# Kernel tuning notes

Hardware: AMD Instinct MI355X
Metric: run time of the kernel (lower is better)

The kernel has to match this reference:

```python
import jax, jax.numpy as jnp
import numpy as np

NUM_RELS = 64
EDGES_PER_REL = 16384
N_NODES = 100000
IN_FEAT = 128
OUT_FEAT = 128
NUM_BASES = 16
E = NUM_RELS * EDGES_PER_REL


def setup_inputs() -> dict:
    key = jax.random.key(0)
    ks = jax.random.split(key, 8)
    feat = jax.random.normal(ks[0], (N_NODES, IN_FEAT), dtype=jnp.float32)
    weight = jax.random.normal(ks[1], (NUM_BASES, IN_FEAT, OUT_FEAT), dtype=jnp.float32) * 0.05
    w_comp = jax.random.normal(ks[2], (NUM_RELS, NUM_BASES), dtype=jnp.float32) * 0.3
    h_bias = jnp.zeros((OUT_FEAT,), dtype=jnp.float32)
    loop_weight = jax.random.normal(ks[3], (IN_FEAT, OUT_FEAT), dtype=jnp.float32) * 0.05
    norm = jax.random.uniform(ks[4], (E, 1), dtype=jnp.float32)
    src = jax.random.randint(ks[5], (E,), 0, N_NODES, dtype=jnp.int32).astype(jnp.int64)
    dst = jax.random.randint(ks[6], (E,), 0, N_NODES, dtype=jnp.int32).astype(jnp.int64)
    # edges are sorted by relation type with uniform per-relation sections
    etypes = jnp.repeat(jnp.arange(NUM_RELS, dtype=jnp.int64), EDGES_PER_REL)
    return {"feat": feat, "weight": weight, "w_comp": w_comp, "h_bias": h_bias,
            "loop_weight": loop_weight, "norm": norm, "src": src, "dst": dst,
            "etypes": etypes, "section": EDGES_PER_REL}


def reference(feat, weight, w_comp, h_bias, loop_weight, norm, src, dst, etypes, section):
    num_rels, num_bases = w_comp.shape
    n_nodes, in_feat = feat.shape
    out_feat = weight.shape[2]
    # basis composition: per-relation weights [R, in, out]
    W = jnp.matmul(w_comp, weight.reshape(num_bases, in_feat * out_feat))
    W = W.reshape(num_rels, in_feat, out_feat)
    # gather per-edge source features (edges sorted by relation, uniform sections)
    h_e = feat[src]                                   # [E, in]
    n_edges = h_e.shape[0]
    h_r = h_e.reshape(num_rels, section, in_feat)     # [R, e_r, in]
    msg = jnp.einsum('rei,rio->reo', h_r, W)          # grouped matmul
    msg = msg.reshape(n_edges, out_feat) * norm       # edge-norm scaling
    # scatter-sum aggregation to destination nodes
    node_repr = jax.ops.segment_sum(msg, dst, num_segments=n_nodes)
    node_repr = node_repr + h_bias + jnp.matmul(feat, loop_weight)
    return jax.nn.relu(node_repr)
```

## Files before the change

### kernel.cpp

```cpp
#include <hip/hip_runtime.h>

#define N_NODES 100000
#define N_PAD 100352
#define NBLK 392
#define IN_FEAT 128
#define OUT_FEAT 128
#define NUM_RELS 64
#define EDGES_PER_REL 16384
#define NUM_BASES 16
#define E_TOTAL (NUM_RELS * EDGES_PER_REL)

typedef __bf16 bf16x8 __attribute__((ext_vector_type(8)));
typedef float floatx4 __attribute__((ext_vector_type(4)));

__global__ __launch_bounds__(256) void compose_w_bf16_kernel(
    const float* __restrict__ weight, const float* __restrict__ w_comp,
    __bf16* __restrict__ Wp) {
  int idx = blockIdx.x * 256 + threadIdx.x;
  int r = idx >> 14;
  int off = idx & 16383;
  int j = off & 7, n = (off >> 3) & 127, kp = off >> 10;
  int k = kp * 8 + j;
  const float* wc = w_comp + r * NUM_BASES;
  float acc = 0.f;
#pragma unroll
  for (int b = 0; b < NUM_BASES; ++b)
    acc += wc[b] * weight[b * 16384 + k * 128 + n];
  Wp[idx] = (__bf16)acc;
}

__global__ __launch_bounds__(256) void pack_loop_w_kernel(
    const float* __restrict__ loop_w, __bf16* __restrict__ Lp) {
  int idx = blockIdx.x * 256 + threadIdx.x;
  int j = idx & 7, n = (idx >> 3) & 127, kp = idx >> 10;
  Lp[idx] = (__bf16)loop_w[(kp * 8 + j) * 128 + n];
}

__global__ __launch_bounds__(256) void compose_w_f32_kernel(
    const float* __restrict__ weight, const float* __restrict__ w_comp,
    float* __restrict__ W) {
  int idx = blockIdx.x * 256 + threadIdx.x;
  int r = idx >> 14;
  int io = idx & 16383;
  const float* wc = w_comp + r * NUM_BASES;
  float acc = 0.f;
#pragma unroll
  for (int b = 0; b < NUM_BASES; ++b)
    acc += wc[b] * weight[b * 16384 + io];
  W[idx] = acc;
}

__global__ __launch_bounds__(256) void init_out_mfma(
    const float* __restrict__ feat, const __bf16* __restrict__ Lp,
    const float* __restrict__ bias, float* __restrict__ out) {
  __shared__ __bf16 A_lds[64 * 136];
  int t = threadIdx.x;
  long base = (long)blockIdx.x * 64;
#pragma unroll
  for (int j = 0; j < 8; ++j) {
    int idx = t + j * 256;
    int e = idx >> 5, k4 = idx & 31;
    long n = base + e;
    float4 v = make_float4(0.f, 0.f, 0.f, 0.f);
    if (n < N_NODES) v = ((const float4*)feat)[n * 32 + k4];
    __bf16 tb[4] = {(__bf16)v.x, (__bf16)v.y, (__bf16)v.z, (__bf16)v.w};
    *(ushort4*)&A_lds[e * 136 + k4 * 4] = *(ushort4*)tb;
  }
  __syncthreads();

  int wave = t >> 6, lane = t & 63;
  int m16 = lane & 15, quad = lane >> 4;
  floatx4 acc[8];
#pragma unroll
  for (int nt = 0; nt < 8; ++nt) acc[nt] = (floatx4){0.f, 0.f, 0.f, 0.f};

  const __bf16* a_base = &A_lds[(wave * 16 + m16) * 136 + quad * 8];
#pragma unroll
  for (int ks = 0; ks < 4; ++ks) {
    bf16x8 a = *(const bf16x8*)(a_base + ks * 32);
    int kp = ks * 4 + quad;
#pragma unroll
    for (int nt = 0; nt < 8; ++nt) {
      bf16x8 b = *(const bf16x8*)(Lp + (kp * 128 + nt * 16 + m16) * 8);
      acc[nt] = __builtin_amdgcn_mfma_f32_16x16x32_bf16(a, b, acc[nt], 0, 0, 0);
    }
  }

  float bv[8];
#pragma unroll
  for (int nt = 0; nt < 8; ++nt) bv[nt] = bias[nt * 16 + m16];
#pragma unroll
  for (int r = 0; r < 4; ++r) {
    long n = base + wave * 16 + quad * 4 + r;
    if (n < N_NODES) {
#pragma unroll
      for (int nt = 0; nt < 8; ++nt)
        out[n * 128 + nt * 16 + m16] = acc[nt][r] + bv[nt];
    }
  }
}

__global__ __launch_bounds__(256) void zero_kernel(int* __restrict__ p) {
  p[blockIdx.x * 256 + threadIdx.x] = 0;
}

__global__ __launch_bounds__(256) void hist8_kernel(
    const int* __restrict__ dst, int* __restrict__ cnt8, int cshift) {
  int e = blockIdx.x * 256 + threadIdx.x;
  int c = e >> cshift;
  atomicAdd(&cnt8[c * N_PAD + dst[e]], 1);
}

__global__ __launch_bounds__(256) void scan1_kernel(
    const int* __restrict__ cnt, int* __restrict__ row,
    int* __restrict__ bsum) {
  __shared__ int s[256];
  int t = threadIdx.x;
  int idx = blockIdx.x * 256 + t;
  int v = cnt[idx];
  s[t] = v;
  __syncthreads();
  for (int o = 1; o < 256; o <<= 1) {
    int x = (t >= o) ? s[t - o] : 0;
    __syncthreads();
    s[t] += x;
    __syncthreads();
  }
  row[idx] = s[t] - v;
  if (t == 255) bsum[blockIdx.x] = s[t];
}

__global__ __launch_bounds__(512) void scan2_kernel(
    const int* __restrict__ bsum, int* __restrict__ boff) {
  __shared__ int s[512];
  int t = threadIdx.x;
  int v = (t < NBLK) ? bsum[blockIdx.x * NBLK + t] : 0;
  s[t] = v;
  __syncthreads();
  for (int o = 1; o < 512; o <<= 1) {
    int x = (t >= o) ? s[t - o] : 0;
    __syncthreads();
    s[t] += x;
    __syncthreads();
  }
  if (t < NBLK) boff[blockIdx.x * NBLK + t] = s[t] - v;
}

__global__ __launch_bounds__(256) void scan3_kernel(
    int* __restrict__ row, const int* __restrict__ boff,
    int* __restrict__ fill) {
  int idx = blockIdx.x * 256 + threadIdx.x;
  int v = row[idx] + boff[blockIdx.x];
  row[idx] = v;
  fill[idx] = v;
}

__global__ __launch_bounds__(256) void scatter_pos_kernel(
    const int* __restrict__ dst, int* __restrict__ fill8,
    int* __restrict__ pos, int cshift) {
  int e = blockIdx.x * 256 + threadIdx.x;
  int c = e >> cshift;
  pos[e] = atomicAdd(&fill8[c * N_PAD + dst[e]], 1);
}

__global__ __launch_bounds__(256) void edge_gemm_mfma(
    const float* __restrict__ feat, const __bf16* __restrict__ Wp,
    const float* __restrict__ norm, const int* __restrict__ src,
    const int* __restrict__ pos, unsigned short* __restrict__ msg, int e_lo) {
  __shared__ __bf16 A_lds[64 * 136];
  __shared__ int s_src[64];
  __shared__ int s_pos[64];
  __shared__ float s_norm[64];
  int t = threadIdx.x;
  long base = (long)e_lo + (long)blockIdx.x * 64;
  int rel = (int)(base >> 14);
  const __bf16* Wr = Wp + (long)rel * (IN_FEAT * OUT_FEAT);

  if (t < 64) {
    s_src[t] = src[base + t];
    s_pos[t] = pos[base + t];
    s_norm[t] = norm[base + t];
  }
  __syncthreads();
#pragma unroll
  for (int j = 0; j < 8; ++j) {
    int idx = t + j * 256;
    int e = idx >> 5, k4 = idx & 31;
    float4 v = ((const float4*)feat)[(long)s_src[e] * 32 + k4];
    __bf16 tb[4] = {(__bf16)v.x, (__bf16)v.y, (__bf16)v.z, (__bf16)v.w};
    *(ushort4*)&A_lds[e * 136 + k4 * 4] = *(ushort4*)tb;
  }
  __syncthreads();

  int wave = t >> 6, lane = t & 63;
  int m16 = lane & 15, quad = lane >> 4;
  floatx4 acc[8];
#pragma unroll
  for (int nt = 0; nt < 8; ++nt) acc[nt] = (floatx4){0.f, 0.f, 0.f, 0.f};

  const __bf16* a_base = &A_lds[(wave * 16 + m16) * 136 + quad * 8];
#pragma unroll
  for (int ks = 0; ks < 4; ++ks) {
    bf16x8 a = *(const bf16x8*)(a_base + ks * 32);
    int kp = ks * 4 + quad;
#pragma unroll
    for (int nt = 0; nt < 8; ++nt) {
      bf16x8 b = *(const bf16x8*)(Wr + (kp * 128 + nt * 16 + m16) * 8);
      acc[nt] = __builtin_amdgcn_mfma_f32_16x16x32_bf16(a, b, acc[nt], 0, 0, 0);
    }
  }

  __syncthreads();
#pragma unroll
  for (int r = 0; r < 4; ++r) {
    int erow = wave * 16 + quad * 4 + r;
    float nm = s_norm[erow];
#pragma unroll
    for (int nt = 0; nt < 8; ++nt)
      A_lds[erow * 136 + nt * 16 + m16] = (__bf16)(acc[nt][r] * nm);
  }
  __syncthreads();
#pragma unroll
  for (int it = 0; it < 4; ++it) {
    int idx = it * 256 + t;
    int row = idx >> 4, seg = idx & 15;
    uint4 v = *(const uint4*)&A_lds[row * 136 + seg * 8];
    *(uint4*)(msg + (long)s_pos[row] * 128 + seg * 8) = v;
  }
}

__global__ __launch_bounds__(256) void gather_csr_kernel(
    const unsigned short* __restrict__ msg, const int* __restrict__ rowc,
    float* __restrict__ out, int do_relu) {
  int wave = threadIdx.x >> 6, lane = threadIdx.x & 63;
  int n = blockIdx.x * 4 + wave;
  if (n >= N_NODES) return;
  int beg = rowc[n], end = rowc[n + 1];
  if (!do_relu && beg == end) return;
  int half = lane >> 5;
  int c4 = lane & 31;
  float s0 = 0.f, s1 = 0.f, s2 = 0.f, s3 = 0.f;
  for (int j = beg + half; j < end; j += 2) {
    uint2 m = *(const uint2*)(msg + (long)j * 128 + c4 * 4);
    s0 += __uint_as_float(m.x << 16);
    s1 += __uint_as_float(m.x & 0xFFFF0000u);
    s2 += __uint_as_float(m.y << 16);
    s3 += __uint_as_float(m.y & 0xFFFF0000u);
  }
  s0 += __shfl_down(s0, 32);
  s1 += __shfl_down(s1, 32);
  s2 += __shfl_down(s2, 32);
  s3 += __shfl_down(s3, 32);
  if (half == 0) {
    float4 o = ((float4*)out)[(long)n * 32 + c4];
    o.x += s0; o.y += s1; o.z += s2; o.w += s3;
    if (do_relu) {
      o.x = fmaxf(o.x, 0.f); o.y = fmaxf(o.y, 0.f);
      o.z = fmaxf(o.z, 0.f); o.w = fmaxf(o.w, 0.f);
    }
    ((float4*)out)[(long)n * 32 + c4] = o;
  }
}

__global__ __launch_bounds__(256) void init_out_f32_kernel(
    const float* __restrict__ feat, const float* __restrict__ loop_w,
    const float* __restrict__ bias, float* __restrict__ out) {
  __shared__ float4 A4[64][32];
  int t = threadIdx.x;
  long base = (long)blockIdx.x * 64;
#pragma unroll
  for (int j = 0; j < 8; ++j) {
    int idx = t + j * 256;
    int e = idx >> 5, k4 = idx & 31;
    long n = base + e;
    float4 v = make_float4(0.f, 0.f, 0.f, 0.f);
    if (n < N_NODES) v = ((const float4*)feat)[n * 32 + k4];
    A4[e][k4] = v;
  }
  __syncthreads();
  int og = t & 31, eg = t >> 5;
  float acc[8][4];
#pragma unroll
  for (int j = 0; j < 8; ++j)
#pragma unroll
    for (int d = 0; d < 4; ++d) acc[j][d] = 0.f;
  const float4* W4 = (const float4*)loop_w;
  for (int k4 = 0; k4 < 32; ++k4) {
    float4 a[8];
#pragma unroll
    for (int j = 0; j < 8; ++j) a[j] = A4[eg * 8 + j][k4];
#pragma unroll
    for (int d = 0; d < 4; ++d) {
      float4 w = W4[(k4 * 4 + d) * 32 + og];
#pragma unroll
      for (int j = 0; j < 8; ++j) {
        float av = ((const float*)&a[j])[d];
        acc[j][0] += av * w.x;
        acc[j][1] += av * w.y;
        acc[j][2] += av * w.z;
        acc[j][3] += av * w.w;
      }
    }
  }
  float4 b = ((const float4*)bias)[og];
#pragma unroll
  for (int j = 0; j < 8; ++j) {
    long n = base + eg * 8 + j;
    if (n < N_NODES) {
      float4 v = make_float4(acc[j][0] + b.x, acc[j][1] + b.y,
                             acc[j][2] + b.z, acc[j][3] + b.w);
      ((float4*)out)[n * 32 + og] = v;
    }
  }
}

__global__ __launch_bounds__(256) void edge_msg_atomic_kernel(
    const float* __restrict__ feat, const float* __restrict__ W,
    const float* __restrict__ norm, const int* __restrict__ src,
    const int* __restrict__ dst, float* __restrict__ out) {
  __shared__ float4 A4[64][32];
  __shared__ int s_src[64];
  __shared__ int s_dst[64];
  __shared__ float s_norm[64];
  int t = threadIdx.x;
  long base = (long)blockIdx.x * 64;
  int rel = blockIdx.x >> 8;
  const float4* Wr4 = (const float4*)(W + (long)rel * IN_FEAT * OUT_FEAT);
  if (t < 64) {
    s_src[t] = src[base + t];
    s_dst[t] = dst[base + t];
    s_norm[t] = norm[base + t];
  }
  __syncthreads();
#pragma unroll
  for (int j = 0; j < 8; ++j) {
    int idx = t + j * 256;
    int e = idx >> 5, k4 = idx & 31;
    A4[e][k4] = ((const float4*)feat)[(long)s_src[e] * 32 + k4];
  }
  __syncthreads();
  int og = t & 31, eg = t >> 5;
  float acc[8][4];
#pragma unroll
  for (int j = 0; j < 8; ++j)
#pragma unroll
    for (int d = 0; d < 4; ++d) acc[j][d] = 0.f;
  for (int k4 = 0; k4 < 32; ++k4) {
    float4 a[8];
#pragma unroll
    for (int j = 0; j < 8; ++j) a[j] = A4[eg * 8 + j][k4];
#pragma unroll
    for (int d = 0; d < 4; ++d) {
      float4 w = Wr4[(k4 * 4 + d) * 32 + og];
#pragma unroll
      for (int j = 0; j < 8; ++j) {
        float av = ((const float*)&a[j])[d];
        acc[j][0] += av * w.x;
        acc[j][1] += av * w.y;
        acc[j][2] += av * w.z;
        acc[j][3] += av * w.w;
      }
    }
  }
#pragma unroll
  for (int j = 0; j < 8; ++j) {
    int e = eg * 8 + j;
    float nm = s_norm[e];
    float* orow = out + (long)s_dst[e] * OUT_FEAT + og * 4;
#pragma unroll
    for (int d = 0; d < 4; ++d) atomicAdd(orow + d, acc[j][d] * nm);
  }
}

__global__ __launch_bounds__(256) void relu_kernel(float* __restrict__ out) {
  int idx = blockIdx.x * 256 + threadIdx.x;
  float4 v = ((const float4*)out)[idx];
  v.x = fmaxf(v.x, 0.f);
  v.y = fmaxf(v.y, 0.f);
  v.z = fmaxf(v.z, 0.f);
  v.w = fmaxf(v.w, 0.f);
  ((float4*)out)[idx] = v;
}

extern "C" void kernel_launch(void* const* d_in, const int* in_sizes, int n_in,
                              void* d_out, int out_size, void* d_ws, size_t ws_size,
                              hipStream_t stream) {
  const float* feat   = (const float*)d_in[0];
  const float* weight = (const float*)d_in[1];
  const float* w_comp = (const float*)d_in[2];
  const float* h_bias = (const float*)d_in[3];
  const float* loop_w = (const float*)d_in[4];
  const float* norm   = (const float*)d_in[5];
  const int*   src    = (const int*)d_in[6];
  const int*   dst    = (const int*)d_in[7];
  float* out = (float*)d_out;

  const size_t SZ_WP  = (size_t)NUM_RELS * IN_FEAT * OUT_FEAT * 2;
  const size_t SZ_LP  = (size_t)IN_FEAT * OUT_FEAT * 2;
  const size_t SZ_POS = (size_t)E_TOTAL * 4;

  int CH = 0;
  {
    const int cands[4] = {32, 16, 8, 4};
    for (int i = 0; i < 4 && CH == 0; ++i) {
      int ch = cands[i], nc = NUM_RELS / ch;
      size_t need = SZ_WP + SZ_LP + SZ_POS + 2 * (size_t)nc * N_PAD * 4 +
                    2 * (size_t)nc * NBLK * 4 +
                    (size_t)ch * EDGES_PER_REL * OUT_FEAT * 2;
      if (ws_size >= need) CH = ch;
    }
  }

  if (CH > 0) {
    const int NC = NUM_RELS / CH;
    const int chunk_edges = CH * EDGES_PER_REL;
    int cshift = 14;
    for (int x = CH; x > 1; x >>= 1) ++cshift;

    char* p = (char*)d_ws;
    __bf16* Wp = (__bf16*)p;                  p += SZ_WP;
    __bf16* Lp = (__bf16*)p;                  p += SZ_LP;
    int* pos  = (int*)p;                      p += SZ_POS;
    int* cnt8 = (int*)p;                      p += (size_t)NC * N_PAD * 4;
    int* row8 = (int*)p;                      p += (size_t)NC * N_PAD * 4;
    int* bsum = (int*)p;                      p += (size_t)NC * NBLK * 4;
    int* boff = (int*)p;                      p += (size_t)NC * NBLK * 4;
    unsigned short* msg = (unsigned short*)p;

    hipLaunchKernelGGL(pack_loop_w_kernel, dim3(16384 / 256), dim3(256), 0,
                       stream, loop_w, Lp);
    hipLaunchKernelGGL(init_out_mfma, dim3((N_NODES + 63) / 64), dim3(256), 0,
                       stream, feat, Lp, h_bias, out);
    hipLaunchKernelGGL(compose_w_bf16_kernel, dim3(NUM_RELS * 16384 / 256),
                       dim3(256), 0, stream, weight, w_comp, Wp);
    hipLaunchKernelGGL(zero_kernel, dim3(NC * NBLK), dim3(256), 0, stream, cnt8);
    hipLaunchKernelGGL(hist8_kernel, dim3(E_TOTAL / 256), dim3(256), 0, stream,
                       dst, cnt8, cshift);
    hipLaunchKernelGGL(scan1_kernel, dim3(NC * NBLK), dim3(256), 0, stream,
                       cnt8, row8, bsum);
    hipLaunchKernelGGL(scan2_kernel, dim3(NC), dim3(512), 0, stream, bsum, boff);
    hipLaunchKernelGGL(scan3_kernel, dim3(NC * NBLK), dim3(256), 0, stream,
                       row8, boff, cnt8);
    hipLaunchKernelGGL(scatter_pos_kernel, dim3(E_TOTAL / 256), dim3(256), 0,
                       stream, dst, cnt8, pos, cshift);

    for (int c = 0; c < NC; ++c) {
      hipLaunchKernelGGL(edge_gemm_mfma, dim3(chunk_edges / 64), dim3(256), 0,
                         stream, feat, Wp, norm, src, pos, msg,
                         c * chunk_edges);
      hipLaunchKernelGGL(gather_csr_kernel, dim3((N_NODES + 3) / 4), dim3(256),
                         0, stream, msg, row8 + (size_t)c * N_PAD, out,
                         (c == NC - 1) ? 1 : 0);
    }
  } else {
    float* W = (float*)d_ws;
    hipLaunchKernelGGL(init_out_f32_kernel, dim3((N_NODES + 63) / 64),
                       dim3(256), 0, stream, feat, loop_w, h_bias, out);
    hipLaunchKernelGGL(compose_w_f32_kernel, dim3(NUM_RELS * 16384 / 256),
                       dim3(256), 0, stream, weight, w_comp, W);
    hipLaunchKernelGGL(edge_msg_atomic_kernel, dim3(E_TOTAL / 64), dim3(256), 0,
                       stream, feat, W, norm, src, dst, out);
    hipLaunchKernelGGL(relu_kernel, dim3((N_NODES * OUT_FEAT / 4) / 256),
                       dim3(256), 0, stream, out);
  }
}
```

Baseline: 460.1 us.

## Fuse edge GEMM with previous chunk's gather in double-buffered launches

Merges the edge GEMM and the CSR gather into one kernel whose blocks are interleaved by role. Each launch runs the GEMM for chunk d while gathering chunk d-1 from a second message buffer, so the two phases overlap on the GPU. The separate scatter_pos pass and its position array are removed by computing slot positions with atomics inside the GEMM blocks. Message stores and loads now use nontemporal hints. Chunks are smaller (max 16 relations) so two buffers fit in the workspace, which means more launches, and the kernel needs registers for both roles, which may lower occupancy.

```diff
diff --git a/kernel.cpp b/kernel.cpp
--- a/kernel.cpp
+++ b/kernel.cpp
@@ -9,9 +9,12 @@
 #define EDGES_PER_REL 16384
 #define NUM_BASES 16
 #define E_TOTAL (NUM_RELS * EDGES_PER_REL)
+#define GATHER_NBLK ((N_NODES + 3) / 4)
 
 typedef __bf16 bf16x8 __attribute__((ext_vector_type(8)));
 typedef float floatx4 __attribute__((ext_vector_type(4)));
+typedef unsigned int uint32x4 __attribute__((ext_vector_type(4)));
+typedef unsigned int uint32x2 __attribute__((ext_vector_type(2)));
 
 __global__ __launch_bounds__(256) void compose_w_bf16_kernel(
     const float* __restrict__ weight, const float* __restrict__ w_comp,
@@ -155,110 +158,115 @@
   fill[idx] = v;
 }
 
-__global__ __launch_bounds__(256) void scatter_pos_kernel(
-    const int* __restrict__ dst, int* __restrict__ fill8,
-    int* __restrict__ pos, int cshift) {
-  int e = blockIdx.x * 256 + threadIdx.x;
-  int c = e >> cshift;
-  pos[e] = atomicAdd(&fill8[c * N_PAD + dst[e]], 1);
-}
-
-__global__ __launch_bounds__(256) void edge_gemm_mfma(
+__global__ __launch_bounds__(256) void fused_gemm_gather(
     const float* __restrict__ feat, const __bf16* __restrict__ Wp,
     const float* __restrict__ norm, const int* __restrict__ src,
-    const int* __restrict__ pos, unsigned short* __restrict__ msg, int e_lo) {
+    const int* __restrict__ dst, int* __restrict__ fill8,
+    const int* __restrict__ rowc, unsigned short* __restrict__ msg_w,
+    const unsigned short* __restrict__ msg_r, float* __restrict__ out,
+    int e_lo, int gemm_nblk, int gather_nblk, int do_relu, int cshift) {
   __shared__ __bf16 A_lds[64 * 136];
   __shared__ int s_src[64];
   __shared__ int s_pos[64];
   __shared__ float s_norm[64];
-  int t = threadIdx.x;
-  long base = (long)e_lo + (long)blockIdx.x * 64;
-  int rel = (int)(base >> 14);
-  const __bf16* Wr = Wp + (long)rel * (IN_FEAT * OUT_FEAT);
-
-  if (t < 64) {
-    s_src[t] = src[base + t];
-    s_pos[t] = pos[base + t];
-    s_norm[t] = norm[base + t];
-  }
-  __syncthreads();
-#pragma unroll
-  for (int j = 0; j < 8; ++j) {
-    int idx = t + j * 256;
-    int e = idx >> 5, k4 = idx & 31;
-    float4 v = ((const float4*)feat)[(long)s_src[e] * 32 + k4];
-    __bf16 tb[4] = {(__bf16)v.x, (__bf16)v.y, (__bf16)v.z, (__bf16)v.w};
-    *(ushort4*)&A_lds[e * 136 + k4 * 4] = *(ushort4*)tb;
-  }
-  __syncthreads();
-
-  int wave = t >> 6, lane = t & 63;
-  int m16 = lane & 15, quad = lane >> 4;
-  floatx4 acc[8];
-#pragma unroll
-  for (int nt = 0; nt < 8; ++nt) acc[nt] = (floatx4){0.f, 0.f, 0.f, 0.f};
-
-  const __bf16* a_base = &A_lds[(wave * 16 + m16) * 136 + quad * 8];
-#pragma unroll
-  for (int ks = 0; ks < 4; ++ks) {
-    bf16x8 a = *(const bf16x8*)(a_base + ks * 32);
-    int kp = ks * 4 + quad;
-#pragma unroll
-    for (int nt = 0; nt < 8; ++nt) {
-      bf16x8 b = *(const bf16x8*)(Wr + (kp * 128 + nt * 16 + m16) * 8);
-      acc[nt] = __builtin_amdgcn_mfma_f32_16x16x32_bf16(a, b, acc[nt], 0, 0, 0);
-    }
-  }
-
-  __syncthreads();
-#pragma unroll
-  for (int r = 0; r < 4; ++r) {
-    int erow = wave * 16 + quad * 4 + r;
-    float nm = s_norm[erow];
-#pragma unroll
-    for (int nt = 0; nt < 8; ++nt)
-      A_lds[erow * 136 + nt * 16 + m16] = (__bf16)(acc[nt][r] * nm);
-  }
-  __syncthreads();
-#pragma unroll
-  for (int it = 0; it < 4; ++it) {
-    int idx = it * 256 + t;
-    int row = idx >> 4, seg = idx & 15;
-    uint4 v = *(const uint4*)&A_lds[row * 136 + seg * 8];
-    *(uint4*)(msg + (long)s_pos[row] * 128 + seg * 8) = v;
-  }
-}
-
-__global__ __launch_bounds__(256) void gather_csr_kernel(
-    const unsigned short* __restrict__ msg, const int* __restrict__ rowc,
-    float* __restrict__ out, int do_relu) {
-  int wave = threadIdx.x >> 6, lane = threadIdx.x & 63;
-  int n = blockIdx.x * 4 + wave;
-  if (n >= N_NODES) return;
-  int beg = rowc[n], end = rowc[n + 1];
-  if (!do_relu && beg == end) return;
-  int half = lane >> 5;
-  int c4 = lane & 31;
-  float s0 = 0.f, s1 = 0.f, s2 = 0.f, s3 = 0.f;
-  for (int j = beg + half; j < end; j += 2) {
-    uint2 m = *(const uint2*)(msg + (long)j * 128 + c4 * 4);
-    s0 += __uint_as_float(m.x << 16);
-    s1 += __uint_as_float(m.x & 0xFFFF0000u);
-    s2 += __uint_as_float(m.y << 16);
-    s3 += __uint_as_float(m.y & 0xFFFF0000u);
-  }
-  s0 += __shfl_down(s0, 32);
-  s1 += __shfl_down(s1, 32);
-  s2 += __shfl_down(s2, 32);
-  s3 += __shfl_down(s3, 32);
-  if (half == 0) {
-    float4 o = ((float4*)out)[(long)n * 32 + c4];
-    o.x += s0; o.y += s1; o.z += s2; o.w += s3;
-    if (do_relu) {
-      o.x = fmaxf(o.x, 0.f); o.y = fmaxf(o.y, 0.f);
-      o.z = fmaxf(o.z, 0.f); o.w = fmaxf(o.w, 0.f);
-    }
-    ((float4*)out)[(long)n * 32 + c4] = o;
+
+  int bx = blockIdx.x;
+  int S = 1 + gather_nblk / (gemm_nblk ? gemm_nblk : 1);
+  int g = bx / S, r0 = bx - g * S;
+  bool is_gemm = (r0 == 0) && (g < gemm_nblk);
+  int t = threadIdx.x;
+
+  if (is_gemm) {
+    long base = (long)e_lo + (long)g * 64;
+    int rel = (int)(base >> 14);
+    int c = e_lo >> cshift;
+    const __bf16* Wr = Wp + (long)rel * (IN_FEAT * OUT_FEAT);
+
+    if (t < 64) {
+      s_src[t] = src[base + t];
+      s_norm[t] = norm[base + t];
+      int d = dst[base + t];
+      s_pos[t] = atomicAdd(&fill8[(long)c * N_PAD + d], 1);
+    }
+    __syncthreads();
+#pragma unroll
+    for (int j = 0; j < 8; ++j) {
+      int idx = t + j * 256;
+      int e = idx >> 5, k4 = idx & 31;
+      float4 v = ((const float4*)feat)[(long)s_src[e] * 32 + k4];
+      __bf16 tb[4] = {(__bf16)v.x, (__bf16)v.y, (__bf16)v.z, (__bf16)v.w};
+      *(ushort4*)&A_lds[e * 136 + k4 * 4] = *(ushort4*)tb;
+    }
+    __syncthreads();
+
+    int wave = t >> 6, lane = t & 63;
+    int m16 = lane & 15, quad = lane >> 4;
+    floatx4 acc[8];
+#pragma unroll
+    for (int nt = 0; nt < 8; ++nt) acc[nt] = (floatx4){0.f, 0.f, 0.f, 0.f};
+
+    const __bf16* a_base = &A_lds[(wave * 16 + m16) * 136 + quad * 8];
+#pragma unroll
+    for (int ks = 0; ks < 4; ++ks) {
+      bf16x8 a = *(const bf16x8*)(a_base + ks * 32);
+      int kp = ks * 4 + quad;
+#pragma unroll
+      for (int nt = 0; nt < 8; ++nt) {
+        bf16x8 b = *(const bf16x8*)(Wr + (kp * 128 + nt * 16 + m16) * 8);
+        acc[nt] = __builtin_amdgcn_mfma_f32_16x16x32_bf16(a, b, acc[nt], 0, 0, 0);
+      }
+    }
+
+    __syncthreads();
+#pragma unroll
+    for (int r = 0; r < 4; ++r) {
+      int erow = wave * 16 + quad * 4 + r;
+      float nm = s_norm[erow];
+#pragma unroll
+      for (int nt = 0; nt < 8; ++nt)
+        A_lds[erow * 136 + nt * 16 + m16] = (__bf16)(acc[nt][r] * nm);
+    }
+    __syncthreads();
+#pragma unroll
+    for (int it = 0; it < 4; ++it) {
+      int idx = it * 256 + t;
+      int row = idx >> 4, seg = idx & 15;
+      uint32x4 v = *(const uint32x4*)&A_lds[row * 136 + seg * 8];
+      __builtin_nontemporal_store(
+          v, (uint32x4*)(msg_w + (long)s_pos[row] * 128 + seg * 8));
+    }
+  } else {
+    int gid = (g < gemm_nblk) ? (g * (S - 1) + (r0 - 1))
+                              : (gemm_nblk * (S - 1) + (bx - gemm_nblk * S));
+    int wave = t >> 6, lane = t & 63;
+    int n = gid * 4 + wave;
+    if (n >= N_NODES) return;
+    int beg = rowc[n], end = rowc[n + 1];
+    if (!do_relu && beg == end) return;
+    int half = lane >> 5;
+    int c4 = lane & 31;
+    float s0 = 0.f, s1 = 0.f, s2 = 0.f, s3 = 0.f;
+    for (int j = beg + half; j < end; j += 2) {
+      uint32x2 m = __builtin_nontemporal_load(
+          (const uint32x2*)(msg_r + (long)j * 128 + c4 * 4));
+      s0 += __uint_as_float(m.x << 16);
+      s1 += __uint_as_float(m.x & 0xFFFF0000u);
+      s2 += __uint_as_float(m.y << 16);
+      s3 += __uint_as_float(m.y & 0xFFFF0000u);
+    }
+    s0 += __shfl_down(s0, 32);
+    s1 += __shfl_down(s1, 32);
+    s2 += __shfl_down(s2, 32);
+    s3 += __shfl_down(s3, 32);
+    if (half == 0) {
+      float4 o = ((float4*)out)[(long)n * 32 + c4];
+      o.x += s0; o.y += s1; o.z += s2; o.w += s3;
+      if (do_relu) {
+        o.x = fmaxf(o.x, 0.f); o.y = fmaxf(o.y, 0.f);
+        o.z = fmaxf(o.z, 0.f); o.w = fmaxf(o.w, 0.f);
+      }
+      ((float4*)out)[(long)n * 32 + c4] = o;
+    }
   }
 }
 
@@ -395,32 +403,33 @@
   const int*   dst    = (const int*)d_in[7];
   float* out = (float*)d_out;
 
-  const size_t SZ_WP  = (size_t)NUM_RELS * IN_FEAT * OUT_FEAT * 2;
-  const size_t SZ_LP  = (size_t)IN_FEAT * OUT_FEAT * 2;
-  const size_t SZ_POS = (size_t)E_TOTAL * 4;
-
-  int CH = 0;
+  const size_t SZ_WP = (size_t)NUM_RELS * IN_FEAT * OUT_FEAT * 2;
+  const size_t SZ_LP = (size_t)IN_FEAT * OUT_FEAT * 2;
+
+  int CH = 0, NBUF = 1;
   {
-    const int cands[4] = {32, 16, 8, 4};
+    const int cands[4] = {16, 8, 4, 2};
     for (int i = 0; i < 4 && CH == 0; ++i) {
       int ch = cands[i], nc = NUM_RELS / ch;
-      size_t need = SZ_WP + SZ_LP + SZ_POS + 2 * (size_t)nc * N_PAD * 4 +
-                    2 * (size_t)nc * NBLK * 4 +
-                    (size_t)ch * EDGES_PER_REL * OUT_FEAT * 2;
-      if (ws_size >= need) CH = ch;
+      size_t per_msg = (size_t)ch * EDGES_PER_REL * OUT_FEAT * 2;
+      size_t fixed = SZ_WP + SZ_LP + 2 * (size_t)nc * N_PAD * 4 +
+                     2 * (size_t)nc * NBLK * 4;
+      if (ws_size >= fixed + 2 * per_msg) { CH = ch; NBUF = 2; }
+      else if (ws_size >= fixed + per_msg) { CH = ch; NBUF = 1; }
     }
   }
 
   if (CH > 0) {
     const int NC = NUM_RELS / CH;
     const int chunk_edges = CH * EDGES_PER_REL;
+    const int gemm_nblk = chunk_edges / 64;
     int cshift = 14;
     for (int x = CH; x > 1; x >>= 1) ++cshift;
+    const size_t CHUNK_SHORTS = (size_t)chunk_edges * OUT_FEAT;
 
     char* p = (char*)d_ws;
     __bf16* Wp = (__bf16*)p;                  p += SZ_WP;
     __bf16* Lp = (__bf16*)p;                  p += SZ_LP;
-    int* pos  = (int*)p;                      p += SZ_POS;
     int* cnt8 = (int*)p;                      p += (size_t)NC * N_PAD * 4;
     int* row8 = (int*)p;                      p += (size_t)NC * N_PAD * 4;
     int* bsum = (int*)p;                      p += (size_t)NC * NBLK * 4;
@@ -441,16 +450,31 @@
     hipLaunchKernelGGL(scan2_kernel, dim3(NC), dim3(512), 0, stream, bsum, boff);
     hipLaunchKernelGGL(scan3_kernel, dim3(NC * NBLK), dim3(256), 0, stream,
                        row8, boff, cnt8);
-    hipLaunchKernelGGL(scatter_pos_kernel, dim3(E_TOTAL / 256), dim3(256), 0,
-                       stream, dst, cnt8, pos, cshift);
-
-    for (int c = 0; c < NC; ++c) {
-      hipLaunchKernelGGL(edge_gemm_mfma, dim3(chunk_edges / 64), dim3(256), 0,
-                         stream, feat, Wp, norm, src, pos, msg,
-                         c * chunk_edges);
-      hipLaunchKernelGGL(gather_csr_kernel, dim3((N_NODES + 3) / 4), dim3(256),
-                         0, stream, msg, row8 + (size_t)c * N_PAD, out,
-                         (c == NC - 1) ? 1 : 0);
+
+    if (NBUF == 2) {
+      for (int d = 0; d <= NC; ++d) {
+        int gn = (d < NC) ? gemm_nblk : 0;
+        int hn = (d >= 1) ? GATHER_NBLK : 0;
+        unsigned short* mw = msg + (size_t)(d & 1) * CHUNK_SHORTS;
+        const unsigned short* mr = msg + (size_t)((d - 1) & 1) * CHUNK_SHORTS;
+        const int* rowc = row8 + (size_t)((d >= 1) ? (d - 1) : 0) * N_PAD;
+        hipLaunchKernelGGL(fused_gemm_gather, dim3(gn + hn), dim3(256), 0,
+                           stream, feat, Wp, norm, src, dst, cnt8, rowc,
+                           mw, mr, out, d * chunk_edges, gn, hn,
+                           (d == NC) ? 1 : 0, cshift);
+      }
+    } else {
+      for (int c = 0; c < NC; ++c) {
+        hipLaunchKernelGGL(fused_gemm_gather, dim3(gemm_nblk), dim3(256), 0,
+                           stream, feat, Wp, norm, src, dst, cnt8, row8,
+                           msg, msg, out, c * chunk_edges, gemm_nblk, 0, 0,
+                           cshift);
+        hipLaunchKernelGGL(fused_gemm_gather, dim3(GATHER_NBLK), dim3(256), 0,
+                           stream, feat, Wp, norm, src, dst, cnt8,
+                           row8 + (size_t)c * N_PAD, msg, msg, out,
+                           c * chunk_edges, 0, GATHER_NBLK,
+                           (c == NC - 1) ? 1 : 0, cshift);
+      }
     }
   } else {
     float* W = (float*)d_ws;
```

Result: slower. 639.1 us (+38.9%).
